# Kernel optimization log

Hardware: AMD Instinct MI355X
Metric: run time of the kernel (lower is better)

The kernel has to match this reference:

```python
import jax, jax.numpy as jnp
import numpy as np

B, Q, C, K = 2, 300, 80, 300
MH = MW = 128
TH = TW = 320


def setup_inputs() -> dict:
    key = jax.random.key(0)
    k1, k2, k3 = jax.random.split(key, 3)
    pred_logits = jax.random.normal(k1, (B, Q, C), dtype=jnp.float32)
    pred_boxes = jax.random.uniform(k2, (B, Q, 4), dtype=jnp.float32)  # cxcywh in [0,1]
    pred_masks = jax.random.normal(k3, (B, Q, MH, MW), dtype=jnp.float32)
    # fixed target size so resize output shape is static (original uses .item() per image)
    orig_target_sizes = jnp.full((B, 2), 320.0, dtype=jnp.float32)  # (w, h)
    return {
        'pred_logits': pred_logits,
        'pred_boxes': pred_boxes,
        'pred_masks': pred_masks,
        'orig_target_sizes': orig_target_sizes,
        'target_h': TH,
        'target_w': TW,
    }


def reference(pred_logits, pred_boxes, pred_masks, orig_target_sizes, target_h, target_w):
    b, q, c = pred_logits.shape
    # cxcywh -> xyxy
    cx, cy, w, h = jnp.split(pred_boxes, 4, axis=-1)
    boxes_xyxy = jnp.concatenate([cx - 0.5 * w, cy - 0.5 * h, cx + 0.5 * w, cy + 0.5 * h], axis=-1)
    # scale factor [w, h, w, h] per image
    scale_fct = jnp.concatenate([orig_target_sizes, orig_target_sizes], axis=1)[:, None, :]  # [B,1,4]
    boxes_abs = boxes_xyxy * scale_fct  # [B,Q,4]

    # focal-loss path: sigmoid scores, topk over flattened (query, class)
    scores_flat = jax.nn.sigmoid(pred_logits).reshape(b, q * c)
    scores, index_flat = jax.lax.top_k(scores_flat, K)  # [B,K]
    labels = index_flat % c
    query_indices = index_flat // c  # [B,K]

    top_boxes = jnp.take_along_axis(boxes_abs, query_indices[:, :, None], axis=1)  # [B,K,4]
    top_masks = jnp.take_along_axis(pred_masks, query_indices[:, :, None, None], axis=1)  # [B,K,MH,MW]

    # bilinear resize, half-pixel centers == torch align_corners=False
    resized = jax.image.resize(top_masks, (b, K, target_h, target_w), method='linear')
    binary_masks = (jax.nn.sigmoid(resized) > 0.5).astype(jnp.float32)

    return scores, labels, top_boxes, binary_masks
```

## Files before the change

kernel.cpp:

```cpp
#include <hip/hip_runtime.h>
#include <stdint.h>

constexpr int Bq = 2;
constexpr int Qn = 300;
constexpr int Cn = 80;
constexpr int Kn = 300;
constexpr int NFLAT = Qn * Cn;
constexpr int MHs = 128;
constexpr int MWs = 128;
constexpr int THs = 320;
constexpr int TWs = 320;

constexpr int OFF_SCORES = 0;
constexpr int OFF_LABELS = Bq * Kn;
constexpr int OFF_BOXES  = 2 * Bq * Kn;
constexpr int OFF_MASKS  = 2 * Bq * Kn + Bq * Kn * 4;

constexpr int TPB = 1024;
constexpr int EPT = (NFLAT + TPB - 1) / TPB;

__global__ __launch_bounds__(TPB) void topk_kernel(
    const float* __restrict__ logits,
    const float* __restrict__ boxes,
    const float* __restrict__ osz,
    float* __restrict__ out,
    int* __restrict__ qidx_ws)
{
    const int b   = blockIdx.x;
    const int tid = threadIdx.x;
    const float* lg = logits + (size_t)b * NFLAT;

    uint32_t bits[EPT];
    #pragma unroll
    for (int j = 0; j < EPT; ++j) {
        int idx = j * TPB + tid;
        bool valid = (idx < NFLAT);
        float x = valid ? lg[idx] : 0.0f;
        float s = 1.0f / (1.0f + expf(-x));
        bits[j] = valid ? __float_as_uint(s) : 0u;
    }

    __shared__ int hist[256];
    __shared__ uint64_t s_pref, s_mask;
    __shared__ int s_r;
    if (tid == 0) { s_pref = 0ull; s_mask = 0ull; s_r = Kn; }
    __syncthreads();

    for (int pass = 0; pass < 8; ++pass) {
        const int shift = 56 - 8 * pass;
        if (tid < 256) hist[tid] = 0;
        __syncthreads();
        const uint64_t pref = s_pref, mask = s_mask;
        #pragma unroll
        for (int j = 0; j < EPT; ++j) {
            int idx = j * TPB + tid;
            if (idx < NFLAT) {
                uint64_t key = ((uint64_t)bits[j] << 32)
                             | (uint64_t)(0xFFFFFFFFu - (uint32_t)idx);
                if ((key & mask) == pref)
                    atomicAdd(&hist[(int)((key >> shift) & 255ull)], 1);
            }
        }
        __syncthreads();
        if (tid == 0) {
            int r = s_r, cum = 0, chosen = 0;
            for (int d = 255; d >= 0; --d) {
                int c = hist[d];
                if (cum + c >= r) { chosen = d; break; }
                cum += c;
            }
            s_r    = r - cum;
            s_pref = pref | ((uint64_t)chosen << shift);
            s_mask = mask | (0xFFull << shift);
        }
        __syncthreads();
    }

    __shared__ unsigned long long sk[Kn];
    __shared__ int cnt;
    if (tid == 0) cnt = 0;
    __syncthreads();
    const uint64_t T = s_pref;
    #pragma unroll
    for (int j = 0; j < EPT; ++j) {
        int idx = j * TPB + tid;
        if (idx < NFLAT) {
            uint64_t key = ((uint64_t)bits[j] << 32)
                         | (uint64_t)(0xFFFFFFFFu - (uint32_t)idx);
            if (key >= T) {
                int p = atomicAdd(&cnt, 1);
                if (p < Kn) sk[p] = key;
            }
        }
    }
    __syncthreads();

    if (tid < Kn) {
        uint64_t my = sk[tid];
        int rank = 0;
        for (int i = 0; i < Kn; ++i) rank += (sk[i] > my);

        uint32_t idx = 0xFFFFFFFFu - (uint32_t)(my & 0xFFFFFFFFull);
        float score  = __uint_as_float((uint32_t)(my >> 32));
        int label = (int)(idx % (uint32_t)Cn);
        int q     = (int)(idx / (uint32_t)Cn);

        out[OFF_SCORES + b * Kn + rank] = score;
        out[OFF_LABELS + b * Kn + rank] = (float)label;

        const float sw = osz[b * 2 + 0];
        const float sh = osz[b * 2 + 1];
        const float* bx = boxes + ((size_t)(b * Qn + q)) * 4;
        float cx = bx[0], cy = bx[1], w = bx[2], h = bx[3];
        float* ob = out + OFF_BOXES + ((size_t)(b * Kn + rank)) * 4;
        ob[0] = (cx - 0.5f * w) * sw;
        ob[1] = (cy - 0.5f * h) * sh;
        ob[2] = (cx + 0.5f * w) * sw;
        ob[3] = (cy + 0.5f * h) * sh;

        qidx_ws[b * Kn + rank] = q;
    }
}

__global__ __launch_bounds__(256) void resize_kernel(
    const float* __restrict__ masks,
    const int* __restrict__ qidx_ws,
    float* __restrict__ out)
{
    const int blk = blockIdx.x;
    const int bk  = blk >> 2;
    const int s   = blk & 3;
    const int tid = threadIdx.x;
    const int b   = bk / Kn;
    const int q   = qidx_ws[bk];
    const int r0  = s * 80;

    __shared__ float  tmp[80 * MWs];
    __shared__ float4 xsw[TWs];
    __shared__ float4 yt[80];

    for (int ox = tid; ox < TWs; ox += 256) {
        float sx  = __fsub_rn(__fdiv_rn(__fadd_rn((float)ox, 0.5f), 2.5f), 0.5f);
        int ix0 = (int)floorf(sx);
        int ix1 = ix0 + 1;
        float wxa = __fsub_rn(1.0f, fabsf(__fsub_rn(sx, (float)ix0)));
        float wxb = __fsub_rn(1.0f, fabsf(__fsub_rn(sx, (float)ix1)));
        if (ix0 < 0)        wxa = 0.0f;
        if (ix1 > MWs - 1)  wxb = 0.0f;
        float sxs = __fadd_rn(wxa, wxb);
        wxa = __fdiv_rn(wxa, sxs);
        wxb = __fdiv_rn(wxb, sxs);
        xsw[(ox >> 2) + 80 * (ox & 3)] =
            make_float4(wxa, wxb,
                        __int_as_float(max(ix0, 0)),
                        __int_as_float(min(ix1, MWs - 1)));
    }
    if (tid < 80) {
        int oy = r0 + tid;
        float sy  = __fsub_rn(__fdiv_rn(__fadd_rn((float)oy, 0.5f), 2.5f), 0.5f);
        int iy0 = (int)floorf(sy);
        int iy1 = iy0 + 1;
        float wya = __fsub_rn(1.0f, fabsf(__fsub_rn(sy, (float)iy0)));
        float wyb = __fsub_rn(1.0f, fabsf(__fsub_rn(sy, (float)iy1)));
        if (iy0 < 0)        wya = 0.0f;
        if (iy1 > MHs - 1)  wyb = 0.0f;
        float ssum = __fadd_rn(wya, wyb);
        wya = __fdiv_rn(wya, ssum);
        wyb = __fdiv_rn(wyb, ssum);
        yt[tid] = make_float4(wya, wyb,
                              __int_as_float(max(iy0, 0)),
                              __int_as_float(min(iy1, MHs - 1)));
    }
    __syncthreads();

    const float* mbase = masks + ((size_t)(b * Qn + q)) * (MHs * MWs);
    for (int i = tid; i < 80 * MWs; i += 256) {
        int oyl = i >> 7;
        int x   = i & (MWs - 1);
        float4 y = yt[oyl];
        int ya = __float_as_int(y.z);
        int yb = __float_as_int(y.w);
        float va = mbase[ya * MWs + x];
        float vb = mbase[yb * MWs + x];
        tmp[i] = __fadd_rn(__fmul_rn(y.x, va), __fmul_rn(y.y, vb));
    }
    __syncthreads();

    float* outm = out + OFF_MASKS + (size_t)bk * (THs * TWs) + (size_t)r0 * TWs;
    for (int qi = tid; qi < (80 * TWs) / 4; qi += 256) {
        int oyl = qi / 80;
        int qm  = qi - oyl * 80;
        const float* row = tmp + oyl * MWs;
        float r4[4];
        #pragma unroll
        for (int t = 0; t < 4; ++t) {
            float4 xw = xsw[qm + 80 * t];
            int c0 = __float_as_int(xw.z);
            int c1 = __float_as_int(xw.w);
            float t0 = row[c0];
            float t1 = row[c1];
            float val = __fadd_rn(__fmul_rn(xw.x, t0), __fmul_rn(xw.y, t1));
            r4[t] = (val > 0.0f) ? 1.0f : 0.0f;
        }
        ((float4*)outm)[qi] = make_float4(r4[0], r4[1], r4[2], r4[3]);
    }
}

extern "C" void kernel_launch(void* const* d_in, const int* in_sizes, int n_in,
                              void* d_out, int out_size, void* d_ws, size_t ws_size,
                              hipStream_t stream) {
    const float* logits = (const float*)d_in[0];
    const float* boxes  = (const float*)d_in[1];
    const float* masks  = (const float*)d_in[2];
    const float* osz    = (const float*)d_in[3];

    float* out = (float*)d_out;
    int* qidx  = (int*)d_ws;

    topk_kernel<<<Bq, TPB, 0, stream>>>(logits, boxes, osz, out, qidx);
    resize_kernel<<<Bq * Kn * 4, 256, 0, stream>>>(masks, qidx, out);
}
```

Baseline: 381.0 us.

## Replace radix top-k with single histogram pass and register-only specialized resize

```diff
diff --git a/kernel.cpp b/kernel.cpp
--- a/kernel.cpp
+++ b/kernel.cpp
@@ -18,6 +18,8 @@
 
 constexpr int TPB = 1024;
 constexpr int EPT = (NFLAT + TPB - 1) / TPB;
+
+typedef float vf4 __attribute__((ext_vector_type(4)));
 
 __global__ __launch_bounds__(TPB) void topk_kernel(
     const float* __restrict__ logits,
@@ -40,89 +42,109 @@
         bits[j] = valid ? __float_as_uint(s) : 0u;
     }
 
-    __shared__ int hist[256];
-    __shared__ uint64_t s_pref, s_mask;
-    __shared__ int s_r;
-    if (tid == 0) { s_pref = 0ull; s_mask = 0ull; s_r = Kn; }
-    __syncthreads();
-
-    for (int pass = 0; pass < 8; ++pass) {
-        const int shift = 56 - 8 * pass;
-        if (tid < 256) hist[tid] = 0;
-        __syncthreads();
-        const uint64_t pref = s_pref, mask = s_mask;
-        #pragma unroll
-        for (int j = 0; j < EPT; ++j) {
-            int idx = j * TPB + tid;
-            if (idx < NFLAT) {
-                uint64_t key = ((uint64_t)bits[j] << 32)
-                             | (uint64_t)(0xFFFFFFFFu - (uint32_t)idx);
-                if ((key & mask) == pref)
-                    atomicAdd(&hist[(int)((key >> shift) & 255ull)], 1);
-            }
-        }
-        __syncthreads();
-        if (tid == 0) {
-            int r = s_r, cum = 0, chosen = 0;
-            for (int d = 255; d >= 0; --d) {
-                int c = hist[d];
-                if (cum + c >= r) { chosen = d; break; }
-                cum += c;
-            }
-            s_r    = r - cum;
-            s_pref = pref | ((uint64_t)chosen << shift);
-            s_mask = mask | (0xFFull << shift);
-        }
-        __syncthreads();
-    }
-
-    __shared__ unsigned long long sk[Kn];
-    __shared__ int cnt;
-    if (tid == 0) cnt = 0;
-    __syncthreads();
-    const uint64_t T = s_pref;
+    __shared__ uint32_t bins[8192];
+    __shared__ int scanA[1024], scanB[1024];
+    __shared__ unsigned long long sk[1024];
+    __shared__ int s_cnt, s_seg, s_B;
+
+    {
+        uint4* b4 = (uint4*)bins;
+        for (int i = tid; i < 8192 / 4; i += TPB) b4[i] = make_uint4(0, 0, 0, 0);
+    }
+    if (tid == 0) s_cnt = 0;
+    __syncthreads();
+
     #pragma unroll
     for (int j = 0; j < EPT; ++j) {
         int idx = j * TPB + tid;
         if (idx < NFLAT) {
-            uint64_t key = ((uint64_t)bits[j] << 32)
-                         | (uint64_t)(0xFFFFFFFFu - (uint32_t)idx);
-            if (key >= T) {
-                int p = atomicAdd(&cnt, 1);
-                if (p < Kn) sk[p] = key;
+            uint32_t bin = bits[j] >> 18;
+            atomicAdd(&bins[bin >> 1], 1u << ((bin & 1u) * 16));
+        }
+    }
+    __syncthreads();
+
+    int sum = 0;
+    #pragma unroll
+    for (int k = 0; k < 8; ++k) {
+        uint32_t v = bins[tid * 8 + k];
+        sum += (int)(v & 0xFFFFu) + (int)(v >> 16);
+    }
+    scanA[tid] = sum;
+    __syncthreads();
+
+    int* src = scanA;
+    int* dst = scanB;
+    for (int d = 1; d < 1024; d <<= 1) {
+        int v = src[tid] + ((tid + d < 1024) ? src[tid + d] : 0);
+        dst[tid] = v;
+        __syncthreads();
+        int* t = src; src = dst; dst = t;
+    }
+
+    int sfx  = src[tid];
+    int sfx1 = (tid < 1023) ? src[tid + 1] : 0;
+    if (sfx >= Kn && sfx1 < Kn) s_seg = tid;
+    __syncthreads();
+
+    if (tid == 0) {
+        int t = s_seg;
+        int cumAbove = (t < 1023) ? src[t + 1] : 0;
+        int B = t * 16;
+        for (int i = 15; i >= 0; --i) {
+            int bin = t * 16 + i;
+            int c = (int)((bins[bin >> 1] >> ((bin & 1) * 16)) & 0xFFFFu);
+            if (cumAbove + c >= Kn) { B = bin; break; }
+            cumAbove += c;
+        }
+        s_B = B;
+    }
+    __syncthreads();
+
+    const uint32_t Bv = (uint32_t)s_B;
+    #pragma unroll
+    for (int j = 0; j < EPT; ++j) {
+        int idx = j * TPB + tid;
+        if (idx < NFLAT && (bits[j] >> 18) >= Bv) {
+            int p = atomicAdd(&s_cnt, 1);
+            if (p < 1024) {
+                sk[p] = ((uint64_t)bits[j] << 32)
+                      | (uint64_t)(0xFFFFFFFFu - (uint32_t)idx);
             }
         }
     }
     __syncthreads();
 
-    if (tid < Kn) {
-        uint64_t my = sk[tid];
+    const int n = min(s_cnt, 1024);
+    if (tid < n) {
+        unsigned long long my = sk[tid];
         int rank = 0;
-        for (int i = 0; i < Kn; ++i) rank += (sk[i] > my);
-
-        uint32_t idx = 0xFFFFFFFFu - (uint32_t)(my & 0xFFFFFFFFull);
-        float score  = __uint_as_float((uint32_t)(my >> 32));
-        int label = (int)(idx % (uint32_t)Cn);
-        int q     = (int)(idx / (uint32_t)Cn);
-
-        out[OFF_SCORES + b * Kn + rank] = score;
-        out[OFF_LABELS + b * Kn + rank] = (float)label;
-
-        const float sw = osz[b * 2 + 0];
-        const float sh = osz[b * 2 + 1];
-        const float* bx = boxes + ((size_t)(b * Qn + q)) * 4;
-        float cx = bx[0], cy = bx[1], w = bx[2], h = bx[3];
-        float* ob = out + OFF_BOXES + ((size_t)(b * Kn + rank)) * 4;
-        ob[0] = (cx - 0.5f * w) * sw;
-        ob[1] = (cy - 0.5f * h) * sh;
-        ob[2] = (cx + 0.5f * w) * sw;
-        ob[3] = (cy + 0.5f * h) * sh;
-
-        qidx_ws[b * Kn + rank] = q;
+        for (int i = 0; i < n; ++i) rank += (sk[i] > my);
+        if (rank < Kn) {
+            uint32_t idx = 0xFFFFFFFFu - (uint32_t)(my & 0xFFFFFFFFull);
+            float score  = __uint_as_float((uint32_t)(my >> 32));
+            int label = (int)(idx % (uint32_t)Cn);
+            int q     = (int)(idx / (uint32_t)Cn);
+
+            out[OFF_SCORES + b * Kn + rank] = score;
+            out[OFF_LABELS + b * Kn + rank] = (float)label;
+
+            const float sw = osz[b * 2 + 0];
+            const float sh = osz[b * 2 + 1];
+            const float* bx = boxes + ((size_t)(b * Qn + q)) * 4;
+            float cx = bx[0], cy = bx[1], w = bx[2], h = bx[3];
+            float* ob = out + OFF_BOXES + ((size_t)(b * Kn + rank)) * 4;
+            ob[0] = (cx - 0.5f * w) * sw;
+            ob[1] = (cy - 0.5f * h) * sh;
+            ob[2] = (cx + 0.5f * w) * sw;
+            ob[3] = (cy + 0.5f * h) * sh;
+
+            qidx_ws[b * Kn + rank] = q;
+        }
     }
 }
 
-__global__ __launch_bounds__(256) void resize_kernel(
+__global__ __launch_bounds__(320) void resize_kernel(
     const float* __restrict__ masks,
     const int* __restrict__ qidx_ws,
     float* __restrict__ out)
@@ -133,77 +155,73 @@
     const int tid = threadIdx.x;
     const int b   = bk / Kn;
     const int q   = qidx_ws[bk];
-    const int r0  = s * 80;
-
-    __shared__ float  tmp[80 * MWs];
-    __shared__ float4 xsw[TWs];
-    __shared__ float4 yt[80];
-
-    for (int ox = tid; ox < TWs; ox += 256) {
-        float sx  = __fsub_rn(__fdiv_rn(__fadd_rn((float)ox, 0.5f), 2.5f), 0.5f);
+
+    const int qm = tid % 80;
+    const int rb = tid / 80;
+
+    const float* M = masks + ((size_t)(b * Qn + q)) * (MHs * MWs);
+
+    float wxa[4], wxb[4];
+    int   c0[4], c1[4];
+    #pragma unroll
+    for (int t = 0; t < 4; ++t) {
+        int ox = 4 * qm + t;
+        float sx = fmaf(0.4f, (float)ox, -0.3f);
         int ix0 = (int)floorf(sx);
-        int ix1 = ix0 + 1;
-        float wxa = __fsub_rn(1.0f, fabsf(__fsub_rn(sx, (float)ix0)));
-        float wxb = __fsub_rn(1.0f, fabsf(__fsub_rn(sx, (float)ix1)));
-        if (ix0 < 0)        wxa = 0.0f;
-        if (ix1 > MWs - 1)  wxb = 0.0f;
-        float sxs = __fadd_rn(wxa, wxb);
-        wxa = __fdiv_rn(wxa, sxs);
-        wxb = __fdiv_rn(wxb, sxs);
-        xsw[(ox >> 2) + 80 * (ox & 3)] =
-            make_float4(wxa, wxb,
-                        __int_as_float(max(ix0, 0)),
-                        __int_as_float(min(ix1, MWs - 1)));
-    }
-    if (tid < 80) {
-        int oy = r0 + tid;
-        float sy  = __fsub_rn(__fdiv_rn(__fadd_rn((float)oy, 0.5f), 2.5f), 0.5f);
-        int iy0 = (int)floorf(sy);
-        int iy1 = iy0 + 1;
-        float wya = __fsub_rn(1.0f, fabsf(__fsub_rn(sy, (float)iy0)));
-        float wyb = __fsub_rn(1.0f, fabsf(__fsub_rn(sy, (float)iy1)));
-        if (iy0 < 0)        wya = 0.0f;
-        if (iy1 > MHs - 1)  wyb = 0.0f;
-        float ssum = __fadd_rn(wya, wyb);
-        wya = __fdiv_rn(wya, ssum);
-        wyb = __fdiv_rn(wyb, ssum);
-        yt[tid] = make_float4(wya, wyb,
-                              __int_as_float(max(iy0, 0)),
-                              __int_as_float(min(iy1, MHs - 1)));
-    }
-    __syncthreads();
-
-    const float* mbase = masks + ((size_t)(b * Qn + q)) * (MHs * MWs);
-    for (int i = tid; i < 80 * MWs; i += 256) {
-        int oyl = i >> 7;
-        int x   = i & (MWs - 1);
-        float4 y = yt[oyl];
-        int ya = __float_as_int(y.z);
-        int yb = __float_as_int(y.w);
-        float va = mbase[ya * MWs + x];
-        float vb = mbase[yb * MWs + x];
-        tmp[i] = __fadd_rn(__fmul_rn(y.x, va), __fmul_rn(y.y, vb));
-    }
-    __syncthreads();
-
-    float* outm = out + OFF_MASKS + (size_t)bk * (THs * TWs) + (size_t)r0 * TWs;
-    for (int qi = tid; qi < (80 * TWs) / 4; qi += 256) {
-        int oyl = qi / 80;
-        int qm  = qi - oyl * 80;
-        const float* row = tmp + oyl * MWs;
-        float r4[4];
+        float fr = sx - (float)ix0;
+        wxb[t] = fr;
+        wxa[t] = 1.0f - fr;
+        c0[t] = max(ix0, 0);
+        c1[t] = min(ix0 + 1, MWs - 1);
+    }
+
+    #define HROW(dst, r)                                                    \
+        {                                                                   \
+            const float* row_ = M + (r) * MWs;                              \
+            _Pragma("unroll")                                               \
+            for (int t = 0; t < 4; ++t)                                     \
+                dst[t] = fmaf(wxa[t], row_[c0[t]], wxb[t] * row_[c1[t]]);   \
+        }
+
+    const int Y0 = 80 * s + 20 * rb;
+    const int M0 = Y0 / 5;
+
+    float h0[4], h1[4], h2[4], h3[4];
+    HROW(h2, max(2 * M0 - 1, 0));
+    HROW(h3, 2 * M0);
+
+    float* outm = out + OFF_MASKS + (size_t)bk * (THs * TWs);
+
+    #pragma unroll
+    for (int g = 0; g < 4; ++g) {
         #pragma unroll
-        for (int t = 0; t < 4; ++t) {
-            float4 xw = xsw[qm + 80 * t];
-            int c0 = __float_as_int(xw.z);
-            int c1 = __float_as_int(xw.w);
-            float t0 = row[c0];
-            float t1 = row[c1];
-            float val = __fadd_rn(__fmul_rn(xw.x, t0), __fmul_rn(xw.y, t1));
-            r4[t] = (val > 0.0f) ? 1.0f : 0.0f;
-        }
-        ((float4*)outm)[qi] = make_float4(r4[0], r4[1], r4[2], r4[3]);
-    }
+        for (int t = 0; t < 4; ++t) { h0[t] = h2[t]; h1[t] = h3[t]; }
+        const int Mg = M0 + g;
+        HROW(h2, 2 * Mg + 1);
+        HROW(h3, min(2 * Mg + 2, MHs - 1));
+
+        float* rp = outm + (size_t)(Y0 + 5 * g) * TWs + 4 * qm;
+        vf4 o;
+
+        #define EMIT(wA, hA, wB, hB, rowoff)                                 \
+            {                                                                \
+                _Pragma("unroll")                                            \
+                for (int t = 0; t < 4; ++t) {                                \
+                    float v = fmaf(wA, hA[t], (wB) * hB[t]);                 \
+                    o[t] = (v > 0.0f) ? 1.0f : 0.0f;                         \
+                }                                                            \
+                __builtin_nontemporal_store(o, (vf4*)(rp + (rowoff) * TWs)); \
+            }
+
+        EMIT(0.3f, h0, 0.7f, h1, 0)
+        EMIT(0.9f, h1, 0.1f, h2, 1)
+        EMIT(0.5f, h1, 0.5f, h2, 2)
+        EMIT(0.1f, h1, 0.9f, h2, 3)
+        EMIT(0.7f, h2, 0.3f, h3, 4)
+
+        #undef EMIT
+    }
+    #undef HROW
 }
 
 extern "C" void kernel_launch(void* const* d_in, const int* in_sizes, int n_in,
@@ -218,5 +236,5 @@
     int* qidx  = (int*)d_ws;
 
     topk_kernel<<<Bq, TPB, 0, stream>>>(logits, boxes, osz, out, qidx);
-    resize_kernel<<<Bq * Kn * 4, 256, 0, stream>>>(masks, qidx, out);
+    resize_kernel<<<Bq * Kn * 4, 320, 0, stream>>>(masks, qidx, out);
 }
```

New measurement: 344.3 us. 1.11x faster.
